# Performance work log

Hardware: AMD Instinct MI355X
Metric: run time of the kernel (lower is better)

## Reference

```python
import jax, jax.numpy as jnp
import numpy as np

N = 8192   # number of nodes / relationships
D = 64     # input_dim == output_dim


def setup_inputs() -> dict:
    key = jax.random.key(0)
    ks = jax.random.split(key, 13)
    s = 0.05
    return {
        "object_features": jax.random.normal(ks[0], (N, D), dtype=jnp.float32),
        "relationship_features": jax.random.normal(ks[1], (N, D), dtype=jnp.float32),
        # sparse-ish 0/1 adjacency, as in the reference usage
        "adjacency_matrix": (jax.random.uniform(ks[2], (N, N)) < 0.05).astype(jnp.float32),
        # nn.Linear params, stored as [in, out] (i.e. torch weight transposed)
        "W_obj": jax.random.normal(ks[3], (D, D), dtype=jnp.float32) * s,
        "b_obj": jax.random.normal(ks[4], (D,), dtype=jnp.float32) * s,
        "W_nobj": jax.random.normal(ks[5], (D, D), dtype=jnp.float32) * s,
        "b_nobj": jax.random.normal(ks[6], (D,), dtype=jnp.float32) * s,
        "W_rel": jax.random.normal(ks[7], (D, D), dtype=jnp.float32) * s,
        "b_rel": jax.random.normal(ks[8], (D,), dtype=jnp.float32) * s,
        "W_skip": jax.random.normal(ks[9], (D, D), dtype=jnp.float32) * s,
        "b_skip": jax.random.normal(ks[10], (D,), dtype=jnp.float32) * s,
        "Wa_w": jax.random.normal(ks[11], (2 * D, 1), dtype=jnp.float32) * s,  # Linear(2D -> 1)
        "Wa_b": jax.random.normal(ks[12], (1,), dtype=jnp.float32) * s,
    }


def reference(object_features, relationship_features, adjacency_matrix,
              W_obj, b_obj, W_nobj, b_nobj, W_rel, b_rel,
              W_skip, b_skip, Wa_w, Wa_b):
    x, r, A = object_features, relationship_features, adjacency_matrix
    d = x.shape[1]

    # message projections (small GEMMs)
    msgs_obj = x @ W_obj + b_obj                      # [N, D]
    msgs_nbr = A.T @ (x @ W_nobj + b_nobj)            # [N, D]
    msgs_rel = r @ W_rel + b_rel                      # [N, D]
    aggregated = msgs_obj + msgs_nbr + msgs_rel       # [N, D]

    # Wa(concat([x_i, r_j])) = x_i @ Wa_w[:d] + r_j @ Wa_w[d:] + Wa_b
    # (avoids materializing the [N, N, 2D] concat the torch code builds)
    sx = x @ Wa_w[:d]                                 # [N, 1] (per row i)
    sr = r @ Wa_w[d:]                                 # [N, 1] (per col j)
    scores = (sx + sr.T + Wa_b) * A                   # [N, N], masked-by-multiply
    attention = jax.nn.softmax(scores, axis=1)        # [N, N]

    # sum_j attn[i, j] * aggregated[i, :]  (exactly the torch broadcast-sum over dim=1)
    attn_agg = jnp.einsum('ij,ik->ik', attention, aggregated)  # [N, D]

    return x @ W_skip + b_skip + attn_agg
```

## Files before the change

kernel.cpp:

```cpp
#include <hip/hip_runtime.h>

typedef __attribute__((ext_vector_type(8))) short short8;
typedef __attribute__((ext_vector_type(4))) float f32x4;
typedef __attribute__((ext_vector_type(4))) unsigned int u32x4;

#define NN 8192
#define DD 64

__device__ inline unsigned short f2bf(float f){
  unsigned b = __float_as_uint(f);
  b = (b + 0x7fffu + ((b >> 16) & 1u)) >> 16;
  return (unsigned short)b;
}


__global__ __launch_bounds__(256) void k_proj(
    const float* __restrict__ x, const float* __restrict__ r,
    const float* __restrict__ Wobj,  const float* __restrict__ bobj,
    const float* __restrict__ Wnobj, const float* __restrict__ bnobj,
    const float* __restrict__ Wrel,  const float* __restrict__ brel,
    const float* __restrict__ Wskip, const float* __restrict__ bskip,
    float* __restrict__ accT, unsigned short* __restrict__ yT)
{
  const int i  = blockIdx.x * 256 + threadIdx.x;
  const int d0 = blockIdx.y * 4;

  float ay[4] = {0.f,0.f,0.f,0.f}, az[4] = {0.f,0.f,0.f,0.f};
  const float4* xp = (const float4*)(x + (size_t)i * DD);
  const float4* rp = (const float4*)(r + (size_t)i * DD);

#pragma unroll
  for (int kb = 0; kb < 4; kb++){
    float xv[16], rv[16];
#pragma unroll
    for (int p = 0; p < 4; p++){
      float4 u = xp[kb*4 + p];
      xv[4*p+0]=u.x; xv[4*p+1]=u.y; xv[4*p+2]=u.z; xv[4*p+3]=u.w;
      float4 v = rp[kb*4 + p];
      rv[4*p+0]=v.x; rv[4*p+1]=v.y; rv[4*p+2]=v.z; rv[4*p+3]=v.w;
    }
#pragma unroll
    for (int kk = 0; kk < 16; kk++){
      const int wb = (kb*16 + kk) * DD + d0;
      const float xk = xv[kk], rk = rv[kk];
#pragma unroll
      for (int t = 0; t < 4; t++){
        ay[t] += xk * Wnobj[wb + t];
        az[t] += xk * Wobj [wb + t];
        az[t] += xk * Wskip[wb + t];
        az[t] += rk * Wrel [wb + t];
      }
    }
  }

#pragma unroll
  for (int t = 0; t < 4; t++){
    ay[t] += bnobj[d0 + t];
    az[t] += bobj[d0 + t] + brel[d0 + t] + bskip[d0 + t];
    yT[(size_t)(d0 + t) * NN + i]   = f2bf(ay[t]);
    accT[(size_t)(d0 + t) * NN + i] = az[t];
  }
}

#define BN 256
#define KSPLIT 16
#define KCH (NN / KSPLIT)
#define KT 32
#define NIT (KCH / KT)
#define ASZ (KT * BN)
#define YPITCH 40
#define YSZ (DD * YPITCH)

__global__ __launch_bounds__(256) void k_spmm(
    const float* __restrict__ A,
    const unsigned short* __restrict__ yT,
    float* __restrict__ part)
{
  __shared__ short Alds[2 * ASZ];
  __shared__ short Ylds[2 * YSZ];

  const int tid  = threadIdx.x;
  const int lane = tid & 63;
  const int wave = tid >> 6;
  const int q    = lane >> 4;
  const int nn   = lane & 15;

  const int j0     = blockIdx.x * BN;
  const int kstart = blockIdx.y * KCH;

  const int c4 = tid & 63;
  const int kr = tid >> 6;
  const int cY = tid & 3;
  const int m  = tid >> 2;

  const float* ap          = A  + (size_t)(kstart + kr) * NN + j0 + c4 * 4;
  const unsigned short* yp = yT + (size_t)m * NN + kstart + cY * 8;

  u32x4 abuf[8]; uint4 ybuf;
  auto gload = [&](){
#pragma unroll
    for (int p = 0; p < 8; p++)
      abuf[p] = __builtin_nontemporal_load((const u32x4*)(ap + (size_t)p * 4 * NN));
    ybuf = *(const uint4*)yp;
    ap += (size_t)KT * NN;
    yp += KT;
  };
  auto stage = [&](int buf){
    short* Ab = &Alds[buf * ASZ];
    short* Yb = &Ylds[buf * YSZ];
#pragma unroll
    for (int p = 0; p < 8; p++){
      const int kk  = kr + p*4;
      const int key = 2 * ((kk >> 3) & 3);
      unsigned lo = (abuf[p][1] & 0xFFFF0000u) | (abuf[p][0] >> 16);
      unsigned hi = (abuf[p][3] & 0xFFFF0000u) | (abuf[p][2] >> 16);
      *(uint2*)(&Ab[kk * BN + (((c4 >> 1) ^ key) * 8) + (c4 & 1) * 4]) =
          make_uint2(lo, hi);
    }
    *(uint4*)(&Yb[m * YPITCH + cY * 8]) = ybuf;
  };

  f32x4 acc[4][4];
#pragma unroll
  for (int a = 0; a < 4; a++)
#pragma unroll
    for (int b = 0; b < 4; b++)
      acc[a][b] = (f32x4){0.f, 0.f, 0.f, 0.f};

  gload();
  stage(0);
  __syncthreads();

  for (int it = 0; it < NIT; ++it){
    if (it + 1 < NIT) gload();
    const short* Ab = &Alds[(it & 1) * ASZ];
    const short* Yb = &Ylds[(it & 1) * YSZ];

    short8 af[4];
#pragma unroll
    for (int mt = 0; mt < 4; mt++)
      af[mt] = *(const short8*)(&Yb[(mt*16 + nn) * YPITCH + q*8]);
#pragma unroll
    for (int nt = 0; nt < 4; nt++){
      const int col = wave * 64 + nt * 16 + nn;
      const short* bp = &Ab[(q*8) * BN + (((col >> 3) ^ (2*q)) * 8) + (col & 7)];
      short8 bf;
#pragma unroll
      for (int jj = 0; jj < 8; jj++) bf[jj] = bp[jj * BN];
#pragma unroll
      for (int mt = 0; mt < 4; mt++)
        acc[mt][nt] = __builtin_amdgcn_mfma_f32_16x16x32_bf16(af[mt], bf, acc[mt][nt], 0, 0, 0);
    }

    if (it + 1 < NIT){
      stage((it + 1) & 1);
      __syncthreads();
    }
  }

  float* pp = part + (size_t)blockIdx.y * DD * NN;
#pragma unroll
  for (int mt = 0; mt < 4; mt++)
#pragma unroll
    for (int nt = 0; nt < 4; nt++)
#pragma unroll
      for (int v = 0; v < 4; v++){
        const int d   = mt * 16 + q * 4 + v;
        const int col = j0 + wave * 64 + nt * 16 + nn;
        pp[(size_t)d * NN + col] = acc[mt][nt][v];
      }
}

__global__ __launch_bounds__(256) void k_out(
    const float* __restrict__ accT, const float* __restrict__ part,
    float* __restrict__ out)
{
  __shared__ float t[64][33];
  const int tid = threadIdx.x;
  const int jb  = blockIdx.x * 32;

#pragma unroll
  for (int rep = 0; rep < 8; rep++){
    const int d = rep * 8 + (tid >> 5);
    const int j = tid & 31;
    const size_t base = (size_t)d * NN + jb + j;
    float s = accT[base];
#pragma unroll
    for (int kb = 0; kb < KSPLIT; kb++)
      s += __builtin_nontemporal_load(part + (size_t)kb * DD * NN + base);
    t[d][j] = s;
  }
  __syncthreads();
#pragma unroll
  for (int rep = 0; rep < 8; rep++){
    const int j = rep * 4 + (tid >> 6);
    const int d = tid & 63;
    out[(size_t)(jb + j) * DD + d] = t[d][j];
  }
}

extern "C" void kernel_launch(void* const* d_in, const int* in_sizes, int n_in,
                              void* d_out, int out_size, void* d_ws, size_t ws_size,
                              hipStream_t stream) {
  const float* x     = (const float*)d_in[0];
  const float* r     = (const float*)d_in[1];
  const float* A     = (const float*)d_in[2];
  const float* Wobj  = (const float*)d_in[3];
  const float* bobj  = (const float*)d_in[4];
  const float* Wnobj = (const float*)d_in[5];
  const float* bnobj = (const float*)d_in[6];
  const float* Wrel  = (const float*)d_in[7];
  const float* brel  = (const float*)d_in[8];
  const float* Wskip = (const float*)d_in[9];
  const float* bskip = (const float*)d_in[10];

  char* ws = (char*)d_ws;
  float* accT        = (float*)ws;
  unsigned short* yT = (unsigned short*)(ws + (size_t)DD*NN*4);
  float* part        = (float*)(ws + 3u*1024*1024);

  k_proj<<<dim3(32, 16), 256, 0, stream>>>(x, r, Wobj, bobj, Wnobj, bnobj,
                                           Wrel, brel, Wskip, bskip, accT, yT);
  k_spmm<<<dim3(NN / BN, KSPLIT), 256, 0, stream>>>(A, yT, part);
  k_out<<<NN / 32, 256, 0, stream>>>(accT, part, (float*)d_out);
}
```

Measured before the change: 408.3 us.

## Replace split-K partial buffers and reduce kernel with atomic adds into output

The projection kernel now writes the skip/obj/rel sum directly into the row-major output. The split-K SpMM kernel atomically adds its partial results into that output instead of writing 16 partial planes. This removes the separate reduction kernel and its 32 MB of partial traffic. In exchange it issues many scattered float atomics (16-way contention per element) and makes the summation order nondeterministic.

```diff
diff --git a/kernel.cpp b/kernel.cpp
--- a/kernel.cpp
+++ b/kernel.cpp
@@ -20,7 +20,7 @@
     const float* __restrict__ Wnobj, const float* __restrict__ bnobj,
     const float* __restrict__ Wrel,  const float* __restrict__ brel,
     const float* __restrict__ Wskip, const float* __restrict__ bskip,
-    float* __restrict__ accT, unsigned short* __restrict__ yT)
+    float* __restrict__ out, unsigned short* __restrict__ yT)
 {
   const int i  = blockIdx.x * 256 + threadIdx.x;
   const int d0 = blockIdx.y * 4;
@@ -57,9 +57,9 @@
   for (int t = 0; t < 4; t++){
     ay[t] += bnobj[d0 + t];
     az[t] += bobj[d0 + t] + brel[d0 + t] + bskip[d0 + t];
-    yT[(size_t)(d0 + t) * NN + i]   = f2bf(ay[t]);
-    accT[(size_t)(d0 + t) * NN + i] = az[t];
+    yT[(size_t)(d0 + t) * NN + i] = f2bf(ay[t]);
   }
+  *(float4*)(out + (size_t)i * DD + d0) = make_float4(az[0], az[1], az[2], az[3]);
 }
 
 #define BN 256
@@ -74,7 +74,7 @@
 __global__ __launch_bounds__(256) void k_spmm(
     const float* __restrict__ A,
     const unsigned short* __restrict__ yT,
-    float* __restrict__ part)
+    float* __restrict__ out)
 {
   __shared__ short Alds[2 * ASZ];
   __shared__ short Ylds[2 * YSZ];
@@ -158,45 +158,17 @@
     }
   }
 
-  float* pp = part + (size_t)blockIdx.y * DD * NN;
 #pragma unroll
   for (int mt = 0; mt < 4; mt++)
 #pragma unroll
-    for (int nt = 0; nt < 4; nt++)
+    for (int nt = 0; nt < 4; nt++){
+      const int col = j0 + wave * 64 + nt * 16 + nn;
 #pragma unroll
       for (int v = 0; v < 4; v++){
-        const int d   = mt * 16 + q * 4 + v;
-        const int col = j0 + wave * 64 + nt * 16 + nn;
-        pp[(size_t)d * NN + col] = acc[mt][nt][v];
+        const int d = mt * 16 + q * 4 + v;
+        atomicAdd(out + (size_t)col * DD + d, acc[mt][nt][v]);
       }
-}
-
-__global__ __launch_bounds__(256) void k_out(
-    const float* __restrict__ accT, const float* __restrict__ part,
-    float* __restrict__ out)
-{
-  __shared__ float t[64][33];
-  const int tid = threadIdx.x;
-  const int jb  = blockIdx.x * 32;
-
-#pragma unroll
-  for (int rep = 0; rep < 8; rep++){
-    const int d = rep * 8 + (tid >> 5);
-    const int j = tid & 31;
-    const size_t base = (size_t)d * NN + jb + j;
-    float s = accT[base];
-#pragma unroll
-    for (int kb = 0; kb < KSPLIT; kb++)
-      s += __builtin_nontemporal_load(part + (size_t)kb * DD * NN + base);
-    t[d][j] = s;
-  }
-  __syncthreads();
-#pragma unroll
-  for (int rep = 0; rep < 8; rep++){
-    const int j = rep * 4 + (tid >> 6);
-    const int d = tid & 63;
-    out[(size_t)(jb + j) * DD + d] = t[d][j];
-  }
+    }
 }
 
 extern "C" void kernel_launch(void* const* d_in, const int* in_sizes, int n_in,
@@ -214,13 +186,10 @@
   const float* Wskip = (const float*)d_in[9];
   const float* bskip = (const float*)d_in[10];
 
-  char* ws = (char*)d_ws;
-  float* accT        = (float*)ws;
-  unsigned short* yT = (unsigned short*)(ws + (size_t)DD*NN*4);
-  float* part        = (float*)(ws + 3u*1024*1024);
+  unsigned short* yT = (unsigned short*)d_ws;
 
   k_proj<<<dim3(32, 16), 256, 0, stream>>>(x, r, Wobj, bobj, Wnobj, bnobj,
-                                           Wrel, brel, Wskip, bskip, accT, yT);
-  k_spmm<<<dim3(NN / BN, KSPLIT), 256, 0, stream>>>(A, yT, part);
-  k_out<<<NN / 32, 256, 0, stream>>>(accT, part, (float*)d_out);
+                                           Wrel, brel, Wskip, bskip,
+                                           (float*)d_out, yT);
+  k_spmm<<<dim3(NN / BN, KSPLIT), 256, 0, stream>>>(A, yT, (float*)d_out);
 }
```

After: 496.2 us. 21.5% more time.
